# Optimization experiments

Measured on AMD Instinct MI355X. Metric: run time of the kernel, lower is better.

## Reference

```python
import jax, jax.numpy as jnp
import numpy as np


def _lstm_cell(x, h, c, Wih, Whh, b):
    # torch gate order: input, forget, cell(g), output
    gates = x @ Wih.T + h @ Whh.T + b  # [B, 4H]
    i, f, g, o = jnp.split(gates, 4, axis=-1)
    i = jax.nn.sigmoid(i)
    f = jax.nn.sigmoid(f)
    g = jnp.tanh(g)
    o = jax.nn.sigmoid(o)
    c = f * c + i * g
    return o * jnp.tanh(c), c


def setup_inputs() -> dict:
    key = jax.random.key(0)
    ks = jax.random.split(key, 20)
    B, Te, Td, X, H = 4096, 168, 24, 8, 64
    s = 0.1  # weight scale for numerical sanity in the AR sampling loop
    return {
        "enc_x": jax.random.normal(ks[0], (B, Te, X), jnp.float32),
        "enc_z": jax.random.uniform(ks[1], (B, Te, 1), jnp.float32),
        "dec_x": jax.random.normal(ks[2], (B, Td, X - 1), jnp.float32),
        "v": jax.random.uniform(ks[3], (B, 1, 1), jnp.float32) + 0.5,  # positive scale
        "eps": jax.random.normal(ks[4], (B, Td, 1), jnp.float32),
        "W_ih0": s * jax.random.normal(ks[5], (4 * H, X), jnp.float32),
        "W_hh0": s * jax.random.normal(ks[6], (4 * H, H), jnp.float32),
        "b0": s * jax.random.normal(ks[7], (4 * H,), jnp.float32),
        "W_ih1": s * jax.random.normal(ks[8], (4 * H, H), jnp.float32),
        "W_hh1": s * jax.random.normal(ks[9], (4 * H, H), jnp.float32),
        "b1": s * jax.random.normal(ks[10], (4 * H,), jnp.float32),
        "W_ih2": s * jax.random.normal(ks[11], (4 * H, H), jnp.float32),
        "W_hh2": s * jax.random.normal(ks[12], (4 * H, H), jnp.float32),
        "b2": s * jax.random.normal(ks[13], (4 * H,), jnp.float32),
        "w_m": s * jax.random.normal(ks[14], (H, 1), jnp.float32),
        "b_m": jnp.zeros((1,), jnp.float32),
        "w_a": s * jax.random.normal(ks[15], (H, 1), jnp.float32),
        "b_a": jnp.zeros((1,), jnp.float32),
    }


def reference(enc_x, enc_z, dec_x, v, eps,
              W_ih0, W_hh0, b0, W_ih1, W_hh1, b1, W_ih2, W_hh2, b2,
              w_m, b_m, w_a, b_a):
    B = enc_x.shape[0]
    H = W_hh0.shape[1]

    def step3(x, h, c):
        h0, c0 = _lstm_cell(x, h[0], c[0], W_ih0, W_hh0, b0)
        h1, c1 = _lstm_cell(h0, h[1], c[1], W_ih1, W_hh1, b1)
        h2, c2 = _lstm_cell(h1, h[2], c[2], W_ih2, W_hh2, b2)
        return (h0, h1, h2), (c0, c1, c2), h2

    z0 = jnp.zeros((B, H), enc_x.dtype)
    h = (z0, z0, z0)
    c = (z0, z0, z0)

    # ---- encoder: 3-layer LSTM over Te steps ----
    def enc_step(carry, x_t):
        h, c = carry
        h, c, _ = step3(x_t, h, c)
        return (h, c), None

    (h, c), _ = jax.lax.scan(enc_step, (h, c), jnp.swapaxes(enc_x, 0, 1))

    vf = v[:, 0, :]                 # [B, 1]
    z = enc_z[:, -1, :] / vf        # [B, 1]

    def dec_step(carry, inp):
        h, c, z = carry
        x_t, e_t = inp              # [B, X-1], [B, 1]
        x = jnp.concatenate([z, x_t], axis=-1)   # [B, X]
        h, c, o = step3(x, h, c)
        m = (o @ w_m + b_m) * vf                  # Gaussian mean, rescaled
        a = jax.nn.softplus(o @ w_a + b_a) * vf   # Gaussian std, rescaled
        zs = m + a * e_t                          # reparameterized sample
        return (h, c, zs / vf), zs

    xs = (jnp.swapaxes(dec_x, 0, 1), jnp.swapaxes(eps, 0, 1))
    _, Z = jax.lax.scan(dec_step, (h, c, z), xs)  # [Td, B, 1]
    return jnp.swapaxes(Z, 0, 1)                  # [B, Td, 1]
```

## Files before the change

kernel.cpp:

```cpp
#include <hip/hip_runtime.h>
#include <math.h>

#define B_TOT 4096
#define TE 168
#define TD 24
#define NWG 256
#define HSTR 72

typedef _Float16 f16;
typedef __attribute__((ext_vector_type(8))) _Float16 f16x8;
typedef __attribute__((ext_vector_type(4))) float f32x4;

#define SCL_S (-1.4426950408889634f)
#define SCL_G (2.885390081777927f)

__global__ __launch_bounds__(256) void pack_kernel(
    const float* __restrict__ Wih0, const float* __restrict__ Whh0,
    const float* __restrict__ Wih1, const float* __restrict__ Whh1,
    const float* __restrict__ Wih2, const float* __restrict__ Whh2,
    f16* __restrict__ pk)
{
    int idx = blockIdx.x * 256 + threadIdx.x;
    int j = idx & 7;
    int t = idx >> 3;
    int ln = t & 63; t >>= 6;
    int c  = t & 3;  t >>= 2;
    int q  = t & 3;  t >>= 2;
    int l  = t % 3;
    int w  = t / 3;
    int row = q * 64 + w * 16 + (ln & 15);
    int k   = c * 32 + ((ln >> 4) << 3) + j;
    float val = 0.f;
    if (l == 0) {
        if (k < 8)                 val = Wih0[row * 8 + k];
        else if (k >= 32 && k < 96) val = Whh0[row * 64 + (k - 32)];
    } else if (l == 1) {
        val = (k < 64) ? Wih1[row * 64 + k] : Whh1[row * 64 + (k - 64)];
    } else {
        val = (k < 64) ? Wih2[row * 64 + k] : Whh2[row * 64 + (k - 64)];
    }
    const float sc = (q == 2) ? SCL_G : SCL_S;
    pk[idx] = (f16)(val * sc);
}

__device__ __forceinline__ float softplusf(float x) {
    float t = fabsf(x) * 1.4426950408889634f;
    float E = __builtin_amdgcn_exp2f(-t);
    float L = __builtin_amdgcn_logf(1.f + E);
    return fmaxf(x, 0.f) + 0.6931471805599453f * L;
}

__global__ __launch_bounds__(768, 2) void lstm_kernel(
    const float* __restrict__ enc_x, const float* __restrict__ enc_z,
    const float* __restrict__ dec_x, const float* __restrict__ v,
    const float* __restrict__ eps,   const f16* __restrict__ pk,
    const float* __restrict__ b0, const float* __restrict__ b1,
    const float* __restrict__ b2,
    const float* __restrict__ w_m, const float* __restrict__ b_m,
    const float* __restrict__ w_a, const float* __restrict__ b_a,
    float* __restrict__ out)
{
    const int tid  = threadIdx.x;
    const int lane = tid & 63;
    const int wv   = (tid >> 6) & 3;
    const int role = tid >> 8;
    const int bg   = blockIdx.x * 16;
    const int m16  = lane & 15;
    const int quad = lane >> 4;

    __shared__ f16 hbuf[2][3][16][HSTR];

    {
        uint* hz = (uint*)&hbuf[0][0][0][0];
        const int HW = 2 * 3 * 16 * HSTR / 2;
        for (int i = tid; i < HW; i += 768) hz[i] = 0u;
    }

    f16x8 wgt[4][4];
#define PKOFF(l, q, c) ((((((size_t)wv * 3 + (l)) * 4 + (q)) * 4 + (c)) * 64 + lane) * 8)
    {
        const f16* pkr = pk + PKOFF(role, 0, 0);
#pragma unroll
        for (int q = 0; q < 4; ++q)
#pragma unroll
            for (int c = 0; c < 4; ++c)
                wgt[c][q] = *(const f16x8*)(pkr + (q * 4 + c) * 64 * 8);
    }
#undef PKOFF

    const int hid_self = wv * 16 + m16;
    f32x4 bsp[4];
    {
        const float* bp = (role == 0) ? b0 : (role == 1) ? b1 : b2;
#pragma unroll
        for (int q = 0; q < 4; ++q) {
            const float sc = (q == 2) ? SCL_G : SCL_S;
            float bv = bp[q * 64 + hid_self] * sc;
            bsp[q] = (f32x4){bv, bv, bv, bv};
        }
    }

    f16* hb = &hbuf[0][0][0][0];
    const int aoff = m16 * HSTR + quad * 8;
    float cst[4] = {};

#define RBAR                                                                  \
    {                                                                         \
        asm volatile("s_waitcnt lgkmcnt(0)" ::: "memory");                    \
        __builtin_amdgcn_s_barrier();                                         \
        asm volatile("" ::: "memory");                                        \
    }

#define PRIO_UP __builtin_amdgcn_s_setprio(1)
#define PRIO_DN __builtin_amdgcn_s_setprio(0)

#define HBASE(pp, l) (hb + ((pp) * 3 + (l)) * (16 * HSTR))
#define MFMA16(af, bf, cf) __builtin_amdgcn_mfma_f32_16x16x32_f16(af, bf, cf, 0, 0, 0)

#define MM_R(P, areg, wi)                                                     \
    {                                                                         \
        P##0 = MFMA16(areg, wgt[wi][0], bsp[0]);                              \
        P##1 = MFMA16(areg, wgt[wi][1], bsp[1]);                              \
        P##2 = MFMA16(areg, wgt[wi][2], bsp[2]);                              \
        P##3 = MFMA16(areg, wgt[wi][3], bsp[3]);                              \
    }
#define MM_RACC(P, areg, wi)                                                  \
    {                                                                         \
        P##0 = MFMA16(areg, wgt[wi][0], P##0);                                \
        P##1 = MFMA16(areg, wgt[wi][1], P##1);                                \
        P##2 = MFMA16(areg, wgt[wi][2], P##2);                                \
        P##3 = MFMA16(areg, wgt[wi][3], P##3);                                \
    }
#define MM_F(P, aptr, wi)                                                     \
    {                                                                         \
        f16x8 af = *(const f16x8*)(aptr);                                     \
        P##0 = MFMA16(af, wgt[wi][0], bsp[0]);                                \
        P##1 = MFMA16(af, wgt[wi][1], bsp[1]);                                \
        P##2 = MFMA16(af, wgt[wi][2], bsp[2]);                                \
        P##3 = MFMA16(af, wgt[wi][3], bsp[3]);                                \
    }
#define MM(P, aptr, wi)                                                       \
    {                                                                         \
        f16x8 af = *(const f16x8*)(aptr);                                     \
        P##0 = MFMA16(af, wgt[wi][0], P##0);                                  \
        P##1 = MFMA16(af, wgt[wi][1], P##1);                                  \
        P##2 = MFMA16(af, wgt[wi][2], P##2);                                  \
        P##3 = MFMA16(af, wgt[wi][3], P##3);                                  \
    }

#define CELL(P, lh, PP)                                                       \
    {                                                                         \
        f16* hw = HBASE(PP, lh) + hid_self;                                   \
        _Pragma("unroll")                                                     \
        for (int r = 0; r < 4; ++r) {                                         \
            float Ei = __builtin_amdgcn_exp2f(P##0[r]);                       \
            float Ef = __builtin_amdgcn_exp2f(P##1[r]);                       \
            float Eg = __builtin_amdgcn_exp2f(P##2[r]);                       \
            float Eo = __builtin_amdgcn_exp2f(P##3[r]);                       \
            float ef1 = 1.f + Ef;                                             \
            float pig = (1.f + Ei) * (1.f + Eg);                              \
            float R   = __builtin_amdgcn_rcpf(pig * ef1);                     \
            float fv  = pig * R;                                              \
            float ig  = (Eg - 1.f) * ef1 * R;                                 \
            float cn  = fmaf(fv, cst[r], ig);                                 \
            cst[r] = cn;                                                      \
            float Ec  = __builtin_amdgcn_exp2f(cn * SCL_G);                   \
            float Roc = __builtin_amdgcn_rcpf((1.f + Eo) * (1.f + Ec));       \
            hw[(quad * 4 + r) * HSTR] = (f16)((Ec - 1.f) * Roc);              \
        }                                                                     \
    }

    const float* xp = enc_x + (size_t)(bg + m16) * (TE * 8);
    f32x4 xa = {}, xb = {};
    f16x8 af_cur = {};
    if (role == 0) {
        xa = *(const f32x4*)xp; xb = *(const f32x4*)(xp + 4);
#pragma unroll
        for (int j = 0; j < 4; ++j) { af_cur[j] = (f16)xa[j]; af_cur[4 + j] = (f16)xb[j]; }
    }

#define ROUND(PP, D0, D1, D2, T0)                                             \
    {                                                                         \
        RBAR;                                                                 \
        f32x4 a0, a1, a2, a3;                                                 \
        if (role == 0) {                                                      \
            if (D0) {                                                         \
                PRIO_UP;                                                      \
                MM_R(a, af_cur, 0);                                           \
                const f16* h0p = HBASE(1 - (PP), 0) + aoff;                   \
                MM(a, h0p, 1);                                                \
                MM(a, h0p + 32, 2);                                           \
                PRIO_DN;                                                      \
                if ((T0) + 1 < TE) {                                          \
                    xa = *(const f32x4*)(xp + (size_t)((T0) + 1) * 8);        \
                    xb = *(const f32x4*)(xp + (size_t)((T0) + 1) * 8 + 4);    \
                }                                                             \
                CELL(a, 0, PP);                                               \
                if ((T0) + 1 < TE) {                                          \
                    _Pragma("unroll")                                         \
                    for (int j = 0; j < 4; ++j) {                             \
                        af_cur[j] = (f16)xa[j]; af_cur[4 + j] = (f16)xb[j];   \
                    }                                                         \
                }                                                             \
            }                                                                 \
        } else if (role == 1) {                                               \
            if (D1) {                                                         \
                PRIO_UP;                                                      \
                const f16* h0p = HBASE(1 - (PP), 0) + aoff;                   \
                const f16* h1p = HBASE(1 - (PP), 1) + aoff;                   \
                MM_F(a, h0p, 0);                                              \
                MM(a, h0p + 32, 1);                                           \
                MM(a, h1p, 2);                                                \
                MM(a, h1p + 32, 3);                                           \
                PRIO_DN;                                                      \
                CELL(a, 1, PP);                                               \
            }                                                                 \
        } else {                                                              \
            if (D2) {                                                         \
                PRIO_UP;                                                      \
                const f16* h1p = HBASE(1 - (PP), 1) + aoff;                   \
                const f16* h2p = HBASE(1 - (PP), 2) + aoff;                   \
                MM_F(a, h1p, 0);                                              \
                MM(a, h1p + 32, 1);                                           \
                MM(a, h2p, 2);                                                \
                MM(a, h2p + 32, 3);                                           \
                PRIO_DN;                                                      \
                CELL(a, 2, PP);                                               \
            }                                                                 \
        }                                                                     \
    }

    ROUND(0, 1, 0, 0, 0)
    ROUND(1, 1, 1, 0, 1)
    for (int t = 2; t < 166; t += 2) {
        ROUND(0, 1, 1, 1, t)
        ROUND(1, 1, 1, 1, t + 1)
    }
    ROUND(0, 1, 1, 1, 166)
    ROUND(1, 1, 1, 1, 167)
    ROUND(0, 0, 1, 1, 168)
    ROUND(1, 0, 0, 1, 169)

    float vf = 0.f, rvf = 0.f, bmv = 0.f, bav = 0.f, zn = 0.f, ep_hold = 0.f;
    float dxr[7] = {};
    f32x4 wmv4[4] = {}, wav4[4] = {};
    if (role == 0) {
        vf  = v[bg + m16];
        rvf = 1.0f / vf;
        bmv = b_m[0]; bav = b_a[0];
        zn  = enc_z[(size_t)(bg + m16) * TE + (TE - 1)] * rvf;
        ep_hold = eps[(size_t)(bg + m16) * TD + 0];
#pragma unroll
        for (int j = 0; j < 7; ++j)
            dxr[j] = dec_x[((size_t)(bg + m16) * TD + 0) * 7 + j];
#pragma unroll
        for (int i = 0; i < 4; ++i) {
            wmv4[i] = *(const f32x4*)(w_m + quad * 16 + 4 * i);
            wav4[i] = *(const f32x4*)(w_a + quad * 16 + 4 * i);
        }
    }

#define HEAD(tOut, ppRead)                                                    \
    {                                                                         \
        const f16* h2p = HBASE(ppRead, 2) + m16 * HSTR + quad * 16;           \
        f16x8 ha = *(const f16x8*)h2p;                                        \
        f16x8 hc = *(const f16x8*)(h2p + 8);                                  \
        float sm = 0.f, sa = 0.f;                                             \
        _Pragma("unroll")                                                     \
        for (int i = 0; i < 4; ++i) {                                         \
            _Pragma("unroll")                                                 \
            for (int j = 0; j < 4; ++j) {                                     \
                float hv = (i < 2) ? (float)ha[i * 4 + j]                     \
                                   : (float)hc[(i - 2) * 4 + j];              \
                sm = fmaf(hv, wmv4[i][j], sm);                                \
                sa = fmaf(hv, wav4[i][j], sa);                                \
            }                                                                 \
        }                                                                     \
        sm += __shfl_xor(sm, 16, 64); sm += __shfl_xor(sm, 32, 64);           \
        sa += __shfl_xor(sa, 16, 64); sa += __shfl_xor(sa, 32, 64);           \
        float mo = (sm + bmv) * vf;                                           \
        float ao = softplusf(sa + bav) * vf;                                  \
        float zs = fmaf(ao, ep_hold, mo);                                     \
        if (tid < 16) out[(size_t)(bg + m16) * TD + (tOut)] = zs;             \
        zn = zs * rvf;                                                        \
    }

    f16x8 pr_a = {}, pr_b = {};
    for (int t = 0; t < TD; ++t) {
        const int PA = t & 1;
        RBAR;
        {
            f32x4 a0, a1, a2, a3;
            if (role == 0) {
                if (t > 0) {
                    HEAD(t - 1, 1 - PA);
                    ep_hold = eps[(size_t)(bg + m16) * TD + t];
                }
                f16x8 af;
                af[0] = (f16)zn;
#pragma unroll
                for (int j = 0; j < 7; ++j) af[1 + j] = (f16)dxr[j];
                MM_R(a, af, 0);
                const f16* h0p = HBASE(1 - PA, 0) + aoff;
                MM(a, h0p, 1);
                MM(a, h0p + 32, 2);
                CELL(a, 0, PA);
                if (t + 1 < TD) {
#pragma unroll
                    for (int j = 0; j < 7; ++j)
                        dxr[j] = dec_x[((size_t)(bg + m16) * TD + (t + 1)) * 7 + j];
                }
            } else if (role == 1) {
                const f16* h1p = HBASE(PA, 1) + aoff;
                pr_a = *(const f16x8*)h1p;
                pr_b = *(const f16x8*)(h1p + 32);
            } else {
                const f16* h2p = HBASE(1 - PA, 2) + aoff;
                pr_a = *(const f16x8*)h2p;
                pr_b = *(const f16x8*)(h2p + 32);
            }
        }
        RBAR;
        if (role == 1) {
            f32x4 a0, a1, a2, a3;
            const f16* h0p = HBASE(PA, 0) + aoff;
            MM_F(a, h0p, 0);
            MM(a, h0p + 32, 1);
            MM_RACC(a, pr_a, 2);
            MM_RACC(a, pr_b, 3);
            CELL(a, 1, 1 - PA);
        }
        RBAR;
        if (role == 2) {
            f32x4 a0, a1, a2, a3;
            const f16* h1p = HBASE(1 - PA, 1) + aoff;
            MM_F(a, h1p, 0);
            MM(a, h1p + 32, 1);
            MM_RACC(a, pr_a, 2);
            MM_RACC(a, pr_b, 3);
            CELL(a, 2, PA);
        }
    }
    RBAR;
    if (role == 0) { HEAD(TD - 1, 1); }

#undef RBAR
#undef PRIO_UP
#undef PRIO_DN
#undef HBASE
#undef MFMA16
#undef MM_R
#undef MM_RACC
#undef MM_F
#undef MM
#undef CELL
#undef ROUND
#undef HEAD
}

extern "C" void kernel_launch(void* const* d_in, const int* in_sizes, int n_in,
                              void* d_out, int out_size, void* d_ws, size_t ws_size,
                              hipStream_t stream) {
    const float* enc_x = (const float*)d_in[0];
    const float* enc_z = (const float*)d_in[1];
    const float* dec_x = (const float*)d_in[2];
    const float* v     = (const float*)d_in[3];
    const float* eps   = (const float*)d_in[4];
    const float* Wih0  = (const float*)d_in[5];
    const float* Whh0  = (const float*)d_in[6];
    const float* b0    = (const float*)d_in[7];
    const float* Wih1  = (const float*)d_in[8];
    const float* Whh1  = (const float*)d_in[9];
    const float* b1    = (const float*)d_in[10];
    const float* Wih2  = (const float*)d_in[11];
    const float* Whh2  = (const float*)d_in[12];
    const float* b2    = (const float*)d_in[13];
    const float* w_m   = (const float*)d_in[14];
    const float* b_m   = (const float*)d_in[15];
    const float* w_a   = (const float*)d_in[16];
    const float* b_a   = (const float*)d_in[17];
    float* out = (float*)d_out;
    f16*   pk  = (f16*)d_ws;

    pack_kernel<<<384, 256, 0, stream>>>(Wih0, Whh0, Wih1, Whh1, Wih2, Whh2, pk);
    lstm_kernel<<<NWG, 768, 0, stream>>>(enc_x, enc_z, dec_x, v, eps, pk,
                                         b0, b1, b2, w_m, b_m, w_a, b_a, out);
}
```

Measured before the change: 296.5 us.

## Use four-slot LDS ring and prefetch next-layer inputs into registers during encoder

Widens the shared hidden-state buffer from two to four slots and reworks the encoder's wavefront pipeline. Layers 1 and 2 now load their input-layer hidden state into registers (hfa/hfb) after their own MFMAs, so those reads are off the critical path of the next round. Recurrent-state reads are issued before the MFMA block instead of inline. This costs more LDS and more registers and makes the slot indexing more intricate, but aims to hide LDS latency behind the compute of each barrier round.

```diff
diff --git a/kernel.cpp b/kernel.cpp
--- a/kernel.cpp
+++ b/kernel.cpp
@@ -68,11 +68,11 @@
     const int m16  = lane & 15;
     const int quad = lane >> 4;
 
-    __shared__ f16 hbuf[2][3][16][HSTR];
+    __shared__ f16 hbuf[4][3][16][HSTR];
 
     {
         uint* hz = (uint*)&hbuf[0][0][0][0];
-        const int HW = 2 * 3 * 16 * HSTR / 2;
+        const int HW = 4 * 3 * 16 * HSTR / 2;
         for (int i = tid; i < HW; i += 768) hz[i] = 0u;
     }
 
@@ -103,6 +103,7 @@
     f16* hb = &hbuf[0][0][0][0];
     const int aoff = m16 * HSTR + quad * 8;
     float cst[4] = {};
+    f16x8 hfa = {}, hfb = {};
 
 #define RBAR                                                                  \
     {                                                                         \
@@ -114,7 +115,7 @@
 #define PRIO_UP __builtin_amdgcn_s_setprio(1)
 #define PRIO_DN __builtin_amdgcn_s_setprio(0)
 
-#define HBASE(pp, l) (hb + ((pp) * 3 + (l)) * (16 * HSTR))
+#define HB(s, l) (hb + ((s) * 3 + (l)) * (16 * HSTR))
 #define MFMA16(af, bf, cf) __builtin_amdgcn_mfma_f32_16x16x32_f16(af, bf, cf, 0, 0, 0)
 
 #define MM_R(P, areg, wi)                                                     \
@@ -131,26 +132,10 @@
         P##2 = MFMA16(areg, wgt[wi][2], P##2);                                \
         P##3 = MFMA16(areg, wgt[wi][3], P##3);                                \
     }
-#define MM_F(P, aptr, wi)                                                     \
-    {                                                                         \
-        f16x8 af = *(const f16x8*)(aptr);                                     \
-        P##0 = MFMA16(af, wgt[wi][0], bsp[0]);                                \
-        P##1 = MFMA16(af, wgt[wi][1], bsp[1]);                                \
-        P##2 = MFMA16(af, wgt[wi][2], bsp[2]);                                \
-        P##3 = MFMA16(af, wgt[wi][3], bsp[3]);                                \
-    }
-#define MM(P, aptr, wi)                                                       \
-    {                                                                         \
-        f16x8 af = *(const f16x8*)(aptr);                                     \
-        P##0 = MFMA16(af, wgt[wi][0], P##0);                                  \
-        P##1 = MFMA16(af, wgt[wi][1], P##1);                                  \
-        P##2 = MFMA16(af, wgt[wi][2], P##2);                                  \
-        P##3 = MFMA16(af, wgt[wi][3], P##3);                                  \
-    }
-
-#define CELL(P, lh, PP)                                                       \
-    {                                                                         \
-        f16* hw = HBASE(PP, lh) + hid_self;                                   \
+
+#define CELL(P, lh, SS)                                                       \
+    {                                                                         \
+        f16* hw = HB(SS, lh) + hid_self;                                      \
         _Pragma("unroll")                                                     \
         for (int r = 0; r < 4; ++r) {                                         \
             float Ei = __builtin_amdgcn_exp2f(P##0[r]);                       \
@@ -171,75 +156,93 @@
     }
 
     const float* xp = enc_x + (size_t)(bg + m16) * (TE * 8);
-    f32x4 xa = {}, xb = {};
-    f16x8 af_cur = {};
     if (role == 0) {
-        xa = *(const f32x4*)xp; xb = *(const f32x4*)(xp + 4);
-#pragma unroll
-        for (int j = 0; j < 4; ++j) { af_cur[j] = (f16)xa[j]; af_cur[4 + j] = (f16)xb[j]; }
-    }
-
-#define ROUND(PP, D0, D1, D2, T0)                                             \
+        f32x4 xa = *(const f32x4*)xp;
+        f32x4 xb = *(const f32x4*)(xp + 4);
+#pragma unroll
+        for (int j = 0; j < 4; ++j) { hfa[j] = (f16)xa[j]; hfa[4 + j] = (f16)xb[j]; }
+    }
+
+#define ROUND(S, D0, D1, P1, D2, P2, T0)                                      \
     {                                                                         \
         RBAR;                                                                 \
         f32x4 a0, a1, a2, a3;                                                 \
         if (role == 0) {                                                      \
             if (D0) {                                                         \
+                const f16* sp = HB((S + 3) & 3, 0) + aoff;                    \
+                f16x8 s0 = *(const f16x8*)sp;                                 \
+                f16x8 s1 = *(const f16x8*)(sp + 32);                          \
                 PRIO_UP;                                                      \
-                MM_R(a, af_cur, 0);                                           \
-                const f16* h0p = HBASE(1 - (PP), 0) + aoff;                   \
-                MM(a, h0p, 1);                                                \
-                MM(a, h0p + 32, 2);                                           \
+                MM_R(a, hfa, 0);                                              \
+                MM_RACC(a, s0, 1);                                            \
+                MM_RACC(a, s1, 2);                                            \
                 PRIO_DN;                                                      \
+                f32x4 xta = {}, xtb = {};                                     \
                 if ((T0) + 1 < TE) {                                          \
-                    xa = *(const f32x4*)(xp + (size_t)((T0) + 1) * 8);        \
-                    xb = *(const f32x4*)(xp + (size_t)((T0) + 1) * 8 + 4);    \
+                    xta = *(const f32x4*)(xp + (size_t)((T0) + 1) * 8);       \
+                    xtb = *(const f32x4*)(xp + (size_t)((T0) + 1) * 8 + 4);   \
                 }                                                             \
-                CELL(a, 0, PP);                                               \
+                CELL(a, 0, S);                                                \
                 if ((T0) + 1 < TE) {                                          \
                     _Pragma("unroll")                                         \
                     for (int j = 0; j < 4; ++j) {                             \
-                        af_cur[j] = (f16)xa[j]; af_cur[4 + j] = (f16)xb[j];   \
+                        hfa[j] = (f16)xta[j]; hfa[4 + j] = (f16)xtb[j];       \
                     }                                                         \
                 }                                                             \
             }                                                                 \
         } else if (role == 1) {                                               \
             if (D1) {                                                         \
+                const f16* sp = HB((S + 1) & 3, 1) + aoff;                    \
+                f16x8 s0 = *(const f16x8*)sp;                                 \
+                f16x8 s1 = *(const f16x8*)(sp + 32);                          \
                 PRIO_UP;                                                      \
-                const f16* h0p = HBASE(1 - (PP), 0) + aoff;                   \
-                const f16* h1p = HBASE(1 - (PP), 1) + aoff;                   \
-                MM_F(a, h0p, 0);                                              \
-                MM(a, h0p + 32, 1);                                           \
-                MM(a, h1p, 2);                                                \
-                MM(a, h1p + 32, 3);                                           \
+                MM_R(a, hfa, 0);                                              \
+                MM_RACC(a, hfb, 1);                                           \
+                MM_RACC(a, s0, 2);                                            \
+                MM_RACC(a, s1, 3);                                            \
                 PRIO_DN;                                                      \
-                CELL(a, 1, PP);                                               \
-            }                                                                 \
+            }                                                                 \
+            if (P1) {                                                         \
+                const f16* pp = HB((S + 3) & 3, 0) + aoff;                    \
+                hfa = *(const f16x8*)pp;                                      \
+                hfb = *(const f16x8*)(pp + 32);                               \
+            }                                                                 \
+            if (D1) CELL(a, 1, (S + 2) & 3);                                  \
         } else {                                                              \
             if (D2) {                                                         \
+                const f16* sp = HB((S + 3) & 3, 2) + aoff;                    \
+                f16x8 s0 = *(const f16x8*)sp;                                 \
+                f16x8 s1 = *(const f16x8*)(sp + 32);                          \
                 PRIO_UP;                                                      \
-                const f16* h1p = HBASE(1 - (PP), 1) + aoff;                   \
-                const f16* h2p = HBASE(1 - (PP), 2) + aoff;                   \
-                MM_F(a, h1p, 0);                                              \
-                MM(a, h1p + 32, 1);                                           \
-                MM(a, h2p, 2);                                                \
-                MM(a, h2p + 32, 3);                                           \
+                MM_R(a, hfa, 0);                                              \
+                MM_RACC(a, hfb, 1);                                           \
+                MM_RACC(a, s0, 2);                                            \
+                MM_RACC(a, s1, 3);                                            \
                 PRIO_DN;                                                      \
-                CELL(a, 2, PP);                                               \
-            }                                                                 \
+            }                                                                 \
+            if (P2) {                                                         \
+                const f16* pp = HB((S + 1) & 3, 1) + aoff;                    \
+                hfa = *(const f16x8*)pp;                                      \
+                hfb = *(const f16x8*)(pp + 32);                               \
+            }                                                                 \
+            if (D2) CELL(a, 2, S);                                            \
         }                                                                     \
     }
 
-    ROUND(0, 1, 0, 0, 0)
-    ROUND(1, 1, 1, 0, 1)
-    for (int t = 2; t < 166; t += 2) {
-        ROUND(0, 1, 1, 1, t)
-        ROUND(1, 1, 1, 1, t + 1)
-    }
-    ROUND(0, 1, 1, 1, 166)
-    ROUND(1, 1, 1, 1, 167)
-    ROUND(0, 0, 1, 1, 168)
-    ROUND(1, 0, 0, 1, 169)
+    ROUND(0, 1, 0, 0, 0, 0, 0)
+    ROUND(1, 1, 0, 1, 0, 0, 1)
+    ROUND(2, 1, 1, 1, 0, 0, 2)
+    ROUND(3, 1, 1, 1, 0, 1, 3)
+    for (int k = 4; k < 168; k += 4) {
+        ROUND(0, 1, 1, 1, 1, 1, k)
+        ROUND(1, 1, 1, 1, 1, 1, k + 1)
+        ROUND(2, 1, 1, 1, 1, 1, k + 2)
+        ROUND(3, 1, 1, 1, 1, 1, k + 3)
+    }
+    ROUND(0, 0, 1, 1, 1, 1, 168)
+    ROUND(1, 0, 1, 0, 1, 1, 169)
+    ROUND(2, 0, 0, 0, 1, 1, 170)
+    ROUND(3, 0, 0, 0, 1, 0, 171)
 
     float vf = 0.f, rvf = 0.f, bmv = 0.f, bav = 0.f, zn = 0.f, ep_hold = 0.f;
     float dxr[7] = {};
@@ -260,9 +263,9 @@
         }
     }
 
-#define HEAD(tOut, ppRead)                                                    \
-    {                                                                         \
-        const f16* h2p = HBASE(ppRead, 2) + m16 * HSTR + quad * 16;           \
+#define HEAD(tOut, SS)                                                        \
+    {                                                                         \
+        const f16* h2p = HB(SS, 2) + m16 * HSTR + quad * 16;                  \
         f16x8 ha = *(const f16x8*)h2p;                                        \
         f16x8 hc = *(const f16x8*)(h2p + 8);                                  \
         float sm = 0.f, sa = 0.f;                                             \
@@ -285,74 +288,78 @@
         zn = zs * rvf;                                                        \
     }
 
-    f16x8 pr_a = {}, pr_b = {};
     for (int t = 0; t < TD; ++t) {
-        const int PA = t & 1;
+        const int sc  = t & 3;
+        const int spv = (t + 3) & 3;
         RBAR;
         {
             f32x4 a0, a1, a2, a3;
             if (role == 0) {
                 if (t > 0) {
-                    HEAD(t - 1, 1 - PA);
+                    HEAD(t - 1, spv);
                     ep_hold = eps[(size_t)(bg + m16) * TD + t];
                 }
                 f16x8 af;
                 af[0] = (f16)zn;
 #pragma unroll
                 for (int j = 0; j < 7; ++j) af[1 + j] = (f16)dxr[j];
+                const f16* h0p = HB(spv, 0) + aoff;
+                f16x8 s0 = *(const f16x8*)h0p;
+                f16x8 s1 = *(const f16x8*)(h0p + 32);
                 MM_R(a, af, 0);
-                const f16* h0p = HBASE(1 - PA, 0) + aoff;
-                MM(a, h0p, 1);
-                MM(a, h0p + 32, 2);
-                CELL(a, 0, PA);
+                MM_RACC(a, s0, 1);
+                MM_RACC(a, s1, 2);
+                CELL(a, 0, sc);
                 if (t + 1 < TD) {
 #pragma unroll
                     for (int j = 0; j < 7; ++j)
                         dxr[j] = dec_x[((size_t)(bg + m16) * TD + (t + 1)) * 7 + j];
                 }
             } else if (role == 1) {
-                const f16* h1p = HBASE(PA, 1) + aoff;
-                pr_a = *(const f16x8*)h1p;
-                pr_b = *(const f16x8*)(h1p + 32);
+                const f16* p = HB(spv, 1) + aoff;
+                hfa = *(const f16x8*)p;
+                hfb = *(const f16x8*)(p + 32);
             } else {
-                const f16* h2p = HBASE(1 - PA, 2) + aoff;
-                pr_a = *(const f16x8*)h2p;
-                pr_b = *(const f16x8*)(h2p + 32);
+                const f16* p = HB(spv, 2) + aoff;
+                hfa = *(const f16x8*)p;
+                hfb = *(const f16x8*)(p + 32);
             }
         }
         RBAR;
         if (role == 1) {
             f32x4 a0, a1, a2, a3;
-            const f16* h0p = HBASE(PA, 0) + aoff;
-            MM_F(a, h0p, 0);
-            MM(a, h0p + 32, 1);
-            MM_RACC(a, pr_a, 2);
-            MM_RACC(a, pr_b, 3);
-            CELL(a, 1, 1 - PA);
+            const f16* h0p = HB(sc, 0) + aoff;
+            f16x8 s0 = *(const f16x8*)h0p;
+            f16x8 s1 = *(const f16x8*)(h0p + 32);
+            MM_R(a, s0, 0);
+            MM_RACC(a, s1, 1);
+            MM_RACC(a, hfa, 2);
+            MM_RACC(a, hfb, 3);
+            CELL(a, 1, sc);
         }
         RBAR;
         if (role == 2) {
             f32x4 a0, a1, a2, a3;
-            const f16* h1p = HBASE(1 - PA, 1) + aoff;
-            MM_F(a, h1p, 0);
-            MM(a, h1p + 32, 1);
-            MM_RACC(a, pr_a, 2);
-            MM_RACC(a, pr_b, 3);
-            CELL(a, 2, PA);
+            const f16* h1p = HB(sc, 1) + aoff;
+            f16x8 s0 = *(const f16x8*)h1p;
+            f16x8 s1 = *(const f16x8*)(h1p + 32);
+            MM_R(a, s0, 0);
+            MM_RACC(a, s1, 1);
+            MM_RACC(a, hfa, 2);
+            MM_RACC(a, hfb, 3);
+            CELL(a, 2, sc);
         }
     }
     RBAR;
-    if (role == 0) { HEAD(TD - 1, 1); }
+    if (role == 0) { HEAD(TD - 1, (TD - 1) & 3); }
 
 #undef RBAR
 #undef PRIO_UP
 #undef PRIO_DN
-#undef HBASE
+#undef HB
 #undef MFMA16
 #undef MM_R
 #undef MM_RACC
-#undef MM_F
-#undef MM
 #undef CELL
 #undef ROUND
 #undef HEAD
```

After: 322.6 us. +8.8%, slower.
